# Performance work log

Measured on AMD Instinct MI355X. Metric: run time of the kernel, lower is better.

The kernel has to match this reference:

```python
import jax, jax.numpy as jnp
import numpy as np

H = 8          # num_heads
EPS = 1e-5     # LayerNorm eps (torch default)


def _layernorm(x, gamma, beta):
    mu = jnp.mean(x, axis=-1, keepdims=True)
    var = jnp.mean(jnp.square(x - mu), axis=-1, keepdims=True)
    return (x - mu) * jax.lax.rsqrt(var + EPS) * gamma + beta


def setup_inputs() -> dict:
    key = jax.random.key(0)
    ks = jax.random.split(key, 20)
    B, S, D, F = 32, 1024, 256, 512
    d = D // H
    s = 1.0 / np.sqrt(D)
    sf = 1.0 / np.sqrt(F)
    inp = {
        "x": jax.random.normal(ks[0], (B, S, D), jnp.float32),
        "hidden": jax.random.normal(ks[1], (B, H, S, d), jnp.float32),
        # attention projections (torch Linear layout: [out, in])
        "Wq": jax.random.uniform(ks[2], (D, D), jnp.float32, -s, s),
        "bq": jnp.zeros((D,), jnp.float32),
        "Wk": jax.random.uniform(ks[3], (D, D), jnp.float32, -s, s),
        "bk": jnp.zeros((D,), jnp.float32),
        "Wv": jax.random.uniform(ks[4], (D, D), jnp.float32, -s, s),
        "bv": jnp.zeros((D,), jnp.float32),
        "Wo": jax.random.uniform(ks[5], (D, D), jnp.float32, -s, s),
        "bo": jnp.zeros((D,), jnp.float32),
        # layernorms
        "g1": jnp.ones((D,), jnp.float32),
        "be1": jnp.zeros((D,), jnp.float32),
        "g2": jnp.ones((D,), jnp.float32),
        "be2": jnp.zeros((D,), jnp.float32),
        # feed-forward
        "W1": jax.random.uniform(ks[6], (F, D), jnp.float32, -s, s),
        "b1": jnp.zeros((F,), jnp.float32),
        "W2": jax.random.uniform(ks[7], (D, F), jnp.float32, -sf, sf),
        "b2": jnp.zeros((D,), jnp.float32),
    }
    return inp


def reference(x, hidden, Wq, bq, Wk, bk, Wv, bv, Wo, bo, g1, be1, g2, be2, W1, b1, W2, b2):
    B, S, D = x.shape
    d = D // H
    scale = 1.0 / np.sqrt(d)

    def split_heads(t):  # [B,S,D] -> [B,H,S,d]
        return t.reshape(B, S, H, d).transpose(0, 2, 1, 3)

    q = split_heads(x @ Wq.T + bq)
    k = split_heads(x @ Wk.T + bk)
    v = split_heads(x @ Wv.T + bv)

    # scores with extra hidden-dependent bias: (q k^T + hidden k^T) / sqrt(d)
    scores = jnp.einsum("bhqd,bhkd->bhqk", q, k) * scale
    scores = scores + jnp.einsum("bhqd,bhkd->bhqk", hidden, k) * scale
    attn = jax.nn.softmax(scores, axis=-1)                 # [B,H,S,S]

    ctx = jnp.einsum("bhqk,bhkd->bhqd", attn, v)           # [B,H,S,d]
    ctx = ctx.transpose(0, 2, 1, 3).reshape(B, S, D)
    attn_out = ctx @ Wo.T + bo

    # x = x + x  (note: residual input discarded, attention output doubled)
    h = attn_out + attn_out
    # FFN with residual (dropout is identity at inference)
    h_norm = _layernorm(h, g1, be1)
    ff = jax.nn.relu(h_norm @ W1.T + b1) @ W2.T + b2
    h = h + ff
    # final: x = x + LayerNorm(x)
    h = h + _layernorm(h, g2, be2)
    return (h, attn)
```

## Files before the change

kernel.cpp:

```cpp
#include <hip/hip_runtime.h>

typedef __attribute__((ext_vector_type(8))) short short8;
typedef __attribute__((ext_vector_type(4))) float f32x4;

constexpr int NB  = 32;
constexpr int NS  = 1024;
constexpr int ND  = 256;
constexpr int NH  = 8;
constexpr int NDH = 32;
constexpr int NF  = 512;
constexpr int NM  = NB * NS;
#define RSD 0.17677669529663687f

static __device__ __forceinline__ ushort f2bf(float f) {
    union { float f; unsigned u; } v; v.f = f;
    unsigned r = v.u + 0x7fffu + ((v.u >> 16) & 1u);
    return (ushort)(r >> 16);
}
static __device__ __forceinline__ float bf2f(ushort u) {
    union { unsigned u; float f; } v; v.u = (unsigned)u << 16; return v.f;
}

__global__ __launch_bounds__(256) void split_hi(
    const float* __restrict__ in, ushort* __restrict__ hi, int n4)
{
    int i = blockIdx.x * 256 + threadIdx.x;
    if (i >= n4) return;
    float4 v = ((const float4*)in)[i];
    ushort4 h;
    h.x = f2bf(v.x); h.y = f2bf(v.y); h.z = f2bf(v.z); h.w = f2bf(v.w);
    ((ushort4*)hi)[i] = h;
}

__global__ __launch_bounds__(256) void split_weights(
    const float* __restrict__ Wq, const float* __restrict__ Wk,
    const float* __restrict__ Wv, const float* __restrict__ Wo,
    const float* __restrict__ W1, const float* __restrict__ W2,
    ushort* __restrict__ whi, ushort* __restrict__ wlo)
{
    const int seg = blockIdx.y;
    const float* src;
    size_t off;
    int n4;
    switch (seg) {
        case 0: src = Wq; off = 0;      n4 = 16384; break;
        case 1: src = Wk; off = 65536;  n4 = 16384; break;
        case 2: src = Wv; off = 131072; n4 = 16384; break;
        case 3: src = Wo; off = 196608; n4 = 16384; break;
        case 4: src = W1; off = 262144; n4 = 32768; break;
        default: src = W2; off = 393216; n4 = 32768; break;
    }
    int i = blockIdx.x * 256 + threadIdx.x;
    if (i >= n4) return;
    float4 v = ((const float4*)src)[i];
    ushort4 h, l;
    h.x = f2bf(v.x); l.x = f2bf(v.x - bf2f(h.x));
    h.y = f2bf(v.y); l.y = f2bf(v.y - bf2f(h.y));
    h.z = f2bf(v.z); l.z = f2bf(v.z - bf2f(h.z));
    h.w = f2bf(v.w); l.w = f2bf(v.w - bf2f(h.w));
    ((ushort4*)(whi + off))[i] = h;
    ((ushort4*)(wlo + off))[i] = l;
}

#define GEMM_CORE(K_, TERMS_)                                                  \
    __shared__ ushort sAh[128 * 40], sAl[128 * 40];                            \
    __shared__ ushort sBh[128 * 40], sBl[128 * 40];                            \
    const int t = threadIdx.x;                                                 \
    const int w = t >> 6, ln = t & 63;                                         \
    const int wr = w >> 1, wc = w & 1;                                         \
    const int col = ln & 15, quad = ln >> 4;                                   \
    const int srow = t >> 1, skb = (t & 1) << 4;                               \
    const ushort* gAh = Ahi + (size_t)(rbase + srow) * (K_) + skb;             \
    const ushort* gAl = (TERMS_ == 3) ? Alo + (size_t)(rbase + srow) * (K_) + skb : gAh; \
    const ushort* gBh = Whi + (size_t)(jbase + srow) * (K_) + skb;             \
    const ushort* gBl = Wlo + (size_t)(jbase + srow) * (K_) + skb;             \
    ushort* wAh = &sAh[srow * 40 + skb];                                       \
    ushort* wAl = &sAl[srow * 40 + skb];                                       \
    ushort* wBh = &sBh[srow * 40 + skb];                                       \
    ushort* wBl = &sBl[srow * 40 + skb];                                       \
    f32x4 acc[4][4] = {};                                                      \
    short8 a0 = *(const short8*)(gAh);                                         \
    short8 a1 = *(const short8*)(gAh + 8);                                     \
    short8 c0 = {}, c1 = {};                                                   \
    if (TERMS_ == 3) { c0 = *(const short8*)(gAl); c1 = *(const short8*)(gAl + 8); } \
    short8 b0 = *(const short8*)(gBh);                                         \
    short8 b1 = *(const short8*)(gBh + 8);                                     \
    short8 d0 = *(const short8*)(gBl);                                         \
    short8 d1 = *(const short8*)(gBl + 8);                                     \
    for (int k0 = 0; k0 < (K_); k0 += 32) {                                    \
        __syncthreads();                                                       \
        *(short8*)wAh = a0; *(short8*)(wAh + 8) = a1;                          \
        if (TERMS_ == 3) { *(short8*)wAl = c0; *(short8*)(wAl + 8) = c1; }     \
        *(short8*)wBh = b0; *(short8*)(wBh + 8) = b1;                          \
        *(short8*)wBl = d0; *(short8*)(wBl + 8) = d1;                          \
        __syncthreads();                                                       \
        if (k0 + 32 < (K_)) {                                                  \
            a0 = *(const short8*)(gAh + k0 + 32);                              \
            a1 = *(const short8*)(gAh + k0 + 40);                              \
            if (TERMS_ == 3) {                                                 \
                c0 = *(const short8*)(gAl + k0 + 32);                          \
                c1 = *(const short8*)(gAl + k0 + 40);                          \
            }                                                                  \
            b0 = *(const short8*)(gBh + k0 + 32);                              \
            b1 = *(const short8*)(gBh + k0 + 40);                              \
            d0 = *(const short8*)(gBl + k0 + 32);                              \
            d1 = *(const short8*)(gBl + k0 + 40);                              \
        }                                                                      \
        short8 af[4], afl[4], bfv[4], bfl[4];                                  \
        _Pragma("unroll")                                                      \
        for (int m = 0; m < 4; ++m) {                                          \
            af[m]  = *(const short8*)&sAh[(wr * 64 + m * 16 + col) * 40 + quad * 8]; \
            if (TERMS_ == 3)                                                   \
                afl[m] = *(const short8*)&sAl[(wr * 64 + m * 16 + col) * 40 + quad * 8]; \
            bfv[m] = *(const short8*)&sBh[(wc * 64 + m * 16 + col) * 40 + quad * 8]; \
            bfl[m] = *(const short8*)&sBl[(wc * 64 + m * 16 + col) * 40 + quad * 8]; \
        }                                                                      \
        _Pragma("unroll")                                                      \
        for (int m = 0; m < 4; ++m)                                            \
            _Pragma("unroll")                                                  \
            for (int n = 0; n < 4; ++n) {                                      \
                acc[m][n] = __builtin_amdgcn_mfma_f32_16x16x32_bf16(af[m],  bfv[n], acc[m][n], 0, 0, 0); \
                acc[m][n] = __builtin_amdgcn_mfma_f32_16x16x32_bf16(af[m],  bfl[n], acc[m][n], 0, 0, 0); \
                if (TERMS_ == 3)                                               \
                    acc[m][n] = __builtin_amdgcn_mfma_f32_16x16x32_bf16(afl[m], bfv[n], acc[m][n], 0, 0, 0); \
            }                                                                  \
    }

template<int TERMS>
__global__ __launch_bounds__(256, 2) void gemm_mfma(
    const ushort* __restrict__ Ahi, const ushort* __restrict__ Alo,
    const ushort* __restrict__ Whi, const ushort* __restrict__ Wlo,
    const float* __restrict__ bias,
    float* __restrict__ outf, ushort* __restrict__ ohi,
    int N, int K, int epi)
{
    const int rbase = blockIdx.y << 7;
    const int jbase = blockIdx.x << 7;
    GEMM_CORE(K, TERMS)

    #pragma unroll
    for (int n = 0; n < 4; ++n) {
        const int cg = jbase + wc * 64 + n * 16 + col;
        const float bs = bias[cg];
        #pragma unroll
        for (int m = 0; m < 4; ++m) {
            #pragma unroll
            for (int r = 0; r < 4; ++r) {
                const int row = rbase + wr * 64 + m * 16 + quad * 4 + r;
                float v = acc[m][n][r] + bs;
                size_t oidx = (size_t)row * N + cg;
                if (epi == 0) {
                    outf[oidx] = 2.f * v;
                } else if (epi == 1) {
                    ohi[oidx] = f2bf(fmaxf(v, 0.f));
                } else {
                    outf[oidx] += v;
                }
            }
        }
    }
}

__global__ __launch_bounds__(256, 2) void gemm_qkv_mfma(
    const ushort* __restrict__ xhi,
    const ushort* __restrict__ whi, const ushort* __restrict__ wlo,
    const float* __restrict__ bq, const float* __restrict__ bk, const float* __restrict__ bv,
    const float* __restrict__ hidden,
    ushort* __restrict__ qhi, ushort* __restrict__ qlo,
    ushort* __restrict__ khi, ushort* __restrict__ klo,
    float* __restrict__ vb)
{
    const int z = blockIdx.z;
    const int rbase = blockIdx.y << 7;
    const int jbase = blockIdx.x << 7;
    const ushort* Ahi = xhi;
    const ushort* Alo = xhi;
    const ushort* Whi = whi + (size_t)z * 65536;
    const ushort* Wlo = wlo + (size_t)z * 65536;
    const float* bias = (z == 0) ? bq : (z == 1) ? bk : bv;
    GEMM_CORE(ND, 2)

    #pragma unroll
    for (int n = 0; n < 4; ++n) {
        const int cg = jbase + wc * 64 + n * 16 + col;
        const float bs = bias[cg];
        const int hh = cg >> 5, dd = cg & 31;
        #pragma unroll
        for (int m = 0; m < 4; ++m) {
            #pragma unroll
            for (int r = 0; r < 4; ++r) {
                const int row = rbase + wr * 64 + m * 16 + quad * 4 + r;
                const int b_i = row >> 10, s_i = row & 1023;
                size_t idx = (((size_t)(b_i * NH + hh)) * NS + s_i) * NDH + dd;
                float v = acc[m][n][r] + bs;
                if (z == 2) {
                    vb[idx] = v;
                } else if (z == 0) {
                    v = (v + hidden[idx]) * RSD;
                    ushort h = f2bf(v);
                    qhi[idx] = h;
                    qlo[idx] = f2bf(v - bf2f(h));
                } else {
                    ushort h = f2bf(v);
                    khi[idx] = h;
                    klo[idx] = f2bf(v - bf2f(h));
                }
            }
        }
    }
}

constexpr int VS  = 136;
constexpr int PST = 136;
__global__ __launch_bounds__(256, 4) void attn_flash(
    const ushort* __restrict__ qhi, const ushort* __restrict__ qlo,
    const ushort* __restrict__ khi, const ushort* __restrict__ klo,
    const float* __restrict__ vb,
    float* __restrict__ attn, ushort* __restrict__ cthi, ushort* __restrict__ ctlo)
{
    __shared__ ushort Vthi[32 * VS];
    __shared__ ushort Vtlo[32 * VS];
    __shared__ ushort Ps[4][16 * PST];
    const int bid = blockIdx.x;
    const int lid = (bid & 7) * 512 + (bid >> 3);
    const int qt = lid & 15, bh = lid >> 4;
    const int q0 = qt << 6;
    const int t = threadIdx.x;
    const int w = t >> 6, ln = t & 63;
    const int col = ln & 15, quad = ln >> 4;
    const int qr0 = q0 + 16 * w;
    ushort* myP = Ps[w];

    const size_t bhbase = (size_t)bh * NS * NDH;
    const size_t aoff = bhbase + (size_t)(qr0 + col) * NDH + quad * 8;
    const short8 ahi = *(const short8*)(qhi + aoff);
    const short8 alo = *(const short8*)(qlo + aoff);

    const float* vbase = vb + bhbase;
    const int sdd = t & 31, skg = (t >> 5) << 4;

    f32x4 acc0 = {0.f, 0.f, 0.f, 0.f}, acc1 = {0.f, 0.f, 0.f, 0.f};
    float S[4] = {0.f, 0.f, 0.f, 0.f};

    for (int k0 = 0; k0 < NS; k0 += 128) {
        __syncthreads();
        ushort hs[16], ls[16];
        #pragma unroll
        for (int c = 0; c < 16; ++c) {
            float xx = vbase[(size_t)(k0 + skg + c) * NDH + sdd];
            ushort h = f2bf(xx);
            hs[c] = h; ls[c] = f2bf(xx - bf2f(h));
        }
        #pragma unroll
        for (int c4 = 0; c4 < 4; ++c4) {
            ushort4 hv = make_ushort4(hs[c4 * 4], hs[c4 * 4 + 1], hs[c4 * 4 + 2], hs[c4 * 4 + 3]);
            ushort4 lv = make_ushort4(ls[c4 * 4], ls[c4 * 4 + 1], ls[c4 * 4 + 2], ls[c4 * 4 + 3]);
            *(ushort4*)&Vthi[sdd * VS + skg + c4 * 4] = hv;
            *(ushort4*)&Vtlo[sdd * VS + skg + c4 * 4] = lv;
        }
        __syncthreads();

        #pragma unroll
        for (int tl = 0; tl < 8; ++tl) {
            const int kk = k0 + tl * 16;
            const size_t boff = bhbase + (size_t)(kk + col) * NDH + quad * 8;
            short8 bhi = *(const short8*)(khi + boff);
            short8 blo = *(const short8*)(klo + boff);
            f32x4 c = {0.f, 0.f, 0.f, 0.f};
            c = __builtin_amdgcn_mfma_f32_16x16x32_bf16(ahi, bhi, c, 0, 0, 0);
            c = __builtin_amdgcn_mfma_f32_16x16x32_bf16(ahi, blo, c, 0, 0, 0);
            c = __builtin_amdgcn_mfma_f32_16x16x32_bf16(alo, bhi, c, 0, 0, 0);
            #pragma unroll
            for (int r = 0; r < 4; ++r) {
                float e = __expf(c[r]);
                S[r] += e;
                myP[(quad * 4 + r) * PST + tl * 16 + col] = f2bf(e);
            }
        }

        #pragma unroll
        for (int sl = 0; sl < 4; ++sl) {
            const int kl = sl * 32 + quad * 8;
            short8 pa = *(const short8*)&myP[col * PST + kl];
            short8 bhi0 = *(const short8*)&Vthi[col * VS + kl];
            short8 blo0 = *(const short8*)&Vtlo[col * VS + kl];
            short8 bhi1 = *(const short8*)&Vthi[(16 + col) * VS + kl];
            short8 blo1 = *(const short8*)&Vtlo[(16 + col) * VS + kl];
            acc0 = __builtin_amdgcn_mfma_f32_16x16x32_bf16(pa, bhi0, acc0, 0, 0, 0);
            acc0 = __builtin_amdgcn_mfma_f32_16x16x32_bf16(pa, blo0, acc0, 0, 0, 0);
            acc1 = __builtin_amdgcn_mfma_f32_16x16x32_bf16(pa, bhi1, acc1, 0, 0, 0);
            acc1 = __builtin_amdgcn_mfma_f32_16x16x32_bf16(pa, blo1, acc1, 0, 0, 0);
        }
    }

    float inv[4];
    #pragma unroll
    for (int r = 0; r < 4; ++r) {
        float s = S[r];
        #pragma unroll
        for (int m = 8; m >= 1; m >>= 1) s += __shfl_xor(s, m, 64);
        inv[r] = 1.f / s;
    }

    const int b_i = bh >> 3, hh = bh & 7;
    const int qrow = qr0 + quad * 4;
    #pragma unroll
    for (int r = 0; r < 4; ++r) {
        size_t base = ((size_t)b_i * NS + qrow + r) * ND + hh * NDH;
        float v0 = acc0[r] * inv[r], v1 = acc1[r] * inv[r];
        ushort h0 = f2bf(v0), h1 = f2bf(v1);
        cthi[base + col]      = h0;
        ctlo[base + col]      = f2bf(v0 - bf2f(h0));
        cthi[base + 16 + col] = h1;
        ctlo[base + 16 + col] = f2bf(v1 - bf2f(h1));
    }

    float* abase = attn + ((size_t)bh * NS + qrow) * NS;
    #pragma unroll 4
    for (int tl = 0; tl < 64; ++tl) {
        const int kk = tl * 16;
        const size_t boff = bhbase + (size_t)(kk + col) * NDH + quad * 8;
        short8 bhi = *(const short8*)(khi + boff);
        short8 blo = *(const short8*)(klo + boff);
        f32x4 c = {0.f, 0.f, 0.f, 0.f};
        c = __builtin_amdgcn_mfma_f32_16x16x32_bf16(ahi, bhi, c, 0, 0, 0);
        c = __builtin_amdgcn_mfma_f32_16x16x32_bf16(ahi, blo, c, 0, 0, 0);
        c = __builtin_amdgcn_mfma_f32_16x16x32_bf16(alo, bhi, c, 0, 0, 0);
        #pragma unroll
        for (int r = 0; r < 4; ++r) {
            float p = __expf(c[r]) * inv[r];
            __builtin_nontemporal_store(p, &abase[(size_t)r * NS + kk + col]);
        }
    }
}

__global__ __launch_bounds__(256) void ln_split(
    const float* __restrict__ x, const float* __restrict__ g,
    const float* __restrict__ be, ushort* __restrict__ ohi)
{
    const int t = threadIdx.x;
    const int wave = t >> 6, lane = t & 63;
    const int row = (blockIdx.x << 2) + wave;
    const float* xr = x + (size_t)row * ND;
    float4 v = *(const float4*)&xr[lane << 2];
    float s = v.x + v.y + v.z + v.w;
    #pragma unroll
    for (int m = 32; m >= 1; m >>= 1) s += __shfl_xor(s, m, 64);
    float mu = s * (1.f / 256.f);
    float dx = v.x - mu, dy = v.y - mu, dz = v.z - mu, dw = v.w - mu;
    float s2 = dx * dx + dy * dy + dz * dz + dw * dw;
    #pragma unroll
    for (int m = 32; m >= 1; m >>= 1) s2 += __shfl_xor(s2, m, 64);
    float rs = rsqrtf(s2 * (1.f / 256.f) + 1e-5f);
    float4 gv = *(const float4*)&g[lane << 2];
    float4 bv = *(const float4*)&be[lane << 2];
    ushort4 h;
    h.x = f2bf(dx * rs * gv.x + bv.x);
    h.y = f2bf(dy * rs * gv.y + bv.y);
    h.z = f2bf(dz * rs * gv.z + bv.z);
    h.w = f2bf(dw * rs * gv.w + bv.w);
    ((ushort4*)ohi)[((size_t)row * ND + (lane << 2)) >> 2] = h;
}

__global__ __launch_bounds__(256) void ln_final(
    const float* __restrict__ x, const float* __restrict__ g,
    const float* __restrict__ be, float* __restrict__ out)
{
    const int t = threadIdx.x;
    const int wave = t >> 6, lane = t & 63;
    const int row = (blockIdx.x << 2) + wave;
    const float* xr = x + (size_t)row * ND;
    float4 v = *(const float4*)&xr[lane << 2];
    float s = v.x + v.y + v.z + v.w;
    #pragma unroll
    for (int m = 32; m >= 1; m >>= 1) s += __shfl_xor(s, m, 64);
    float mu = s * (1.f / 256.f);
    float dx = v.x - mu, dy = v.y - mu, dz = v.z - mu, dw = v.w - mu;
    float s2 = dx * dx + dy * dy + dz * dz + dw * dw;
    #pragma unroll
    for (int m = 32; m >= 1; m >>= 1) s2 += __shfl_xor(s2, m, 64);
    float rs = rsqrtf(s2 * (1.f / 256.f) + 1e-5f);
    float4 gv = *(const float4*)&g[lane << 2];
    float4 bv = *(const float4*)&be[lane << 2];
    float4 o;
    o.x = dx * rs * gv.x + bv.x + v.x;
    o.y = dy * rs * gv.y + bv.y + v.y;
    o.z = dz * rs * gv.z + bv.z + v.z;
    o.w = dw * rs * gv.w + bv.w + v.w;
    *(float4*)&out[(size_t)row * ND + (lane << 2)] = o;
}

extern "C" void kernel_launch(void* const* d_in, const int* in_sizes, int n_in,
                              void* d_out, int out_size, void* d_ws, size_t ws_size,
                              hipStream_t stream)
{
    const float* x      = (const float*)d_in[0];
    const float* hidden = (const float*)d_in[1];
    const float* Wq = (const float*)d_in[2];
    const float* bq = (const float*)d_in[3];
    const float* Wk = (const float*)d_in[4];
    const float* bk = (const float*)d_in[5];
    const float* Wv = (const float*)d_in[6];
    const float* bv = (const float*)d_in[7];
    const float* Wo = (const float*)d_in[8];
    const float* bo = (const float*)d_in[9];
    const float* g1  = (const float*)d_in[10];
    const float* be1 = (const float*)d_in[11];
    const float* g2  = (const float*)d_in[12];
    const float* be2 = (const float*)d_in[13];
    const float* W1 = (const float*)d_in[14];
    const float* b1 = (const float*)d_in[15];
    const float* W2 = (const float*)d_in[16];
    const float* b2 = (const float*)d_in[17];

    float* out  = (float*)d_out;
    float* attn = out + (size_t)NM * ND;

    float* ws = (float*)d_ws;
    ushort* xhi  = (ushort*)ws;
    ushort* qhi  = (ushort*)(ws + 8388608);
    ushort* qlo  = (ushort*)(ws + 12582912);
    ushort* khi  = (ushort*)(ws + 16777216);
    ushort* klo  = (ushort*)(ws + 20971520);
    float*  vbuf = ws + 25165824;
    ushort* cthi = (ushort*)ws;
    ushort* ctlo = (ushort*)(ws + 4194304);
    float*  hbuf = ws + 33554432;
    ushort* hnhi = (ushort*)(ws + 8388608);
    ushort* ffhi = (ushort*)(ws + 16777216);
    ushort* whi  = (ushort*)(ws + 41943040);
    ushort* wlo  = (ushort*)(ws + 42205184);

    split_weights<<<dim3(128, 6), 256, 0, stream>>>(Wq, Wk, Wv, Wo, W1, W2, whi, wlo);
    split_hi<<<8192, 256, 0, stream>>>(x, xhi, 2097152);

    gemm_qkv_mfma<<<dim3(2, 256, 3), 256, 0, stream>>>(
        xhi, whi, wlo, bq, bk, bv, hidden, qhi, qlo, khi, klo, vbuf);
    attn_flash<<<dim3(4096), 256, 0, stream>>>(
        qhi, qlo, khi, klo, vbuf, attn, cthi, ctlo);
    gemm_mfma<3><<<dim3(2, 256), 256, 0, stream>>>(
        cthi, ctlo, whi + 196608, wlo + 196608, bo, hbuf, nullptr, ND, ND, 0);
    ln_split<<<NM / 4, 256, 0, stream>>>(hbuf, g1, be1, hnhi);
    gemm_mfma<2><<<dim3(4, 256), 256, 0, stream>>>(
        hnhi, nullptr, whi + 262144, wlo + 262144, b1, nullptr, ffhi, NF, ND, 1);
    gemm_mfma<2><<<dim3(2, 256), 256, 0, stream>>>(
        ffhi, nullptr, whi + 393216, wlo + 393216, b2, hbuf, nullptr, ND, NF, 2);
    ln_final<<<NM / 4, 256, 0, stream>>>(hbuf, g2, be2, out);
}
```

Before: 541.2 us.

## Fuse LayerNorms into output-projection and FFN2 GEMM epilogues

Replaces the O-projection GEMM plus ln_split, and the FFN2 GEMM plus ln_final, with two new GEMM kernels. Each block computes a full 64x256 row tile so the LayerNorm row statistics can be reduced in registers with shuffles. This removes two elementwise kernels and their round trips of the hidden buffer through global memory. In exchange, each kernel launches only 512 blocks with large accumulator arrays and bigger shared tiles, which may lower occupancy. Variance now uses E[x²]-mu², which is less accurate than the previous two-pass form.

Result: faster. 525.3 us (-2.9%).

```diff
diff --git a/kernel.cpp b/kernel.cpp
--- a/kernel.cpp
+++ b/kernel.cpp
@@ -210,6 +210,189 @@
     }
 }
 
+__global__ __launch_bounds__(256, 2) void gemm_oproj_ln(
+    const ushort* __restrict__ Ahi, const ushort* __restrict__ Alo,
+    const ushort* __restrict__ Whi, const ushort* __restrict__ Wlo,
+    const float* __restrict__ bias, const float* __restrict__ g,
+    const float* __restrict__ be,
+    float* __restrict__ hbuf, ushort* __restrict__ hnhi)
+{
+    __shared__ ushort sAh[64 * 40], sAl[64 * 40];
+    __shared__ ushort sBh[256 * 40], sBl[256 * 40];
+    const int t = threadIdx.x;
+    const int w = t >> 6, ln = t & 63;
+    const int col = ln & 15, quad = ln >> 4;
+    const int rbase = blockIdx.x << 6;
+    const int arow = t >> 2, akb = (t & 3) << 3;
+    const ushort* gAh = Ahi + (size_t)(rbase + arow) * ND + akb;
+    const ushort* gAl = Alo + (size_t)(rbase + arow) * ND + akb;
+    const ushort* gBh = Whi + (size_t)t * ND;
+    const ushort* gBl = Wlo + (size_t)t * ND;
+    ushort* wAh = &sAh[arow * 40 + akb];
+    ushort* wAl = &sAl[arow * 40 + akb];
+    ushort* wBh = &sBh[t * 40];
+    ushort* wBl = &sBl[t * 40];
+
+    f32x4 acc[16] = {};
+    short8 a0 = *(const short8*)gAh;
+    short8 c0 = *(const short8*)gAl;
+    short8 b0 = *(const short8*)(gBh),      b1 = *(const short8*)(gBh + 8);
+    short8 b2v = *(const short8*)(gBh + 16), b3 = *(const short8*)(gBh + 24);
+    short8 d0 = *(const short8*)(gBl),      d1 = *(const short8*)(gBl + 8);
+    short8 d2v = *(const short8*)(gBl + 16), d3 = *(const short8*)(gBl + 24);
+
+    for (int k0 = 0; k0 < ND; k0 += 32) {
+        __syncthreads();
+        *(short8*)wAh = a0; *(short8*)wAl = c0;
+        *(short8*)(wBh + 0) = b0;  *(short8*)(wBh + 8) = b1;
+        *(short8*)(wBh + 16) = b2v; *(short8*)(wBh + 24) = b3;
+        *(short8*)(wBl + 0) = d0;  *(short8*)(wBl + 8) = d1;
+        *(short8*)(wBl + 16) = d2v; *(short8*)(wBl + 24) = d3;
+        __syncthreads();
+        if (k0 + 32 < ND) {
+            a0 = *(const short8*)(gAh + k0 + 32);
+            c0 = *(const short8*)(gAl + k0 + 32);
+            b0 = *(const short8*)(gBh + k0 + 32); b1 = *(const short8*)(gBh + k0 + 40);
+            b2v = *(const short8*)(gBh + k0 + 48); b3 = *(const short8*)(gBh + k0 + 56);
+            d0 = *(const short8*)(gBl + k0 + 32); d1 = *(const short8*)(gBl + k0 + 40);
+            d2v = *(const short8*)(gBl + k0 + 48); d3 = *(const short8*)(gBl + k0 + 56);
+        }
+        short8 af  = *(const short8*)&sAh[(w * 16 + col) * 40 + quad * 8];
+        short8 afl = *(const short8*)&sAl[(w * 16 + col) * 40 + quad * 8];
+        #pragma unroll
+        for (int n = 0; n < 16; ++n) {
+            short8 bv = *(const short8*)&sBh[(n * 16 + col) * 40 + quad * 8];
+            short8 bl = *(const short8*)&sBl[(n * 16 + col) * 40 + quad * 8];
+            acc[n] = __builtin_amdgcn_mfma_f32_16x16x32_bf16(af,  bv, acc[n], 0, 0, 0);
+            acc[n] = __builtin_amdgcn_mfma_f32_16x16x32_bf16(af,  bl, acc[n], 0, 0, 0);
+            acc[n] = __builtin_amdgcn_mfma_f32_16x16x32_bf16(afl, bv, acc[n], 0, 0, 0);
+        }
+    }
+
+    const int row0 = rbase + w * 16 + quad * 4;
+    float s[4] = {}, s2[4] = {};
+    #pragma unroll
+    for (int n = 0; n < 16; ++n) {
+        float bs = bias[n * 16 + col];
+        #pragma unroll
+        for (int r = 0; r < 4; ++r) {
+            float hv = 2.f * (acc[n][r] + bs);
+            acc[n][r] = hv;
+            s[r] += hv; s2[r] += hv * hv;
+            hbuf[(size_t)(row0 + r) * ND + n * 16 + col] = hv;
+        }
+    }
+    float mu[4], rsd[4];
+    #pragma unroll
+    for (int r = 0; r < 4; ++r) {
+        #pragma unroll
+        for (int m = 8; m >= 1; m >>= 1) {
+            s[r]  += __shfl_xor(s[r],  m, 64);
+            s2[r] += __shfl_xor(s2[r], m, 64);
+        }
+        mu[r] = s[r] * (1.f / 256.f);
+        float var = s2[r] * (1.f / 256.f) - mu[r] * mu[r];
+        rsd[r] = rsqrtf(var + 1e-5f);
+    }
+    #pragma unroll
+    for (int n = 0; n < 16; ++n) {
+        float gv = g[n * 16 + col], bv = be[n * 16 + col];
+        #pragma unroll
+        for (int r = 0; r < 4; ++r)
+            hnhi[(size_t)(row0 + r) * ND + n * 16 + col] =
+                f2bf((acc[n][r] - mu[r]) * rsd[r] * gv + bv);
+    }
+}
+
+__global__ __launch_bounds__(256, 2) void gemm_ffn2_ln(
+    const ushort* __restrict__ Ahi,
+    const ushort* __restrict__ Whi, const ushort* __restrict__ Wlo,
+    const float* __restrict__ bias, const float* __restrict__ g,
+    const float* __restrict__ be,
+    const float* __restrict__ hbuf, float* __restrict__ out)
+{
+    __shared__ ushort sAh[64 * 40];
+    __shared__ ushort sBh[256 * 40], sBl[256 * 40];
+    const int t = threadIdx.x;
+    const int w = t >> 6, ln = t & 63;
+    const int col = ln & 15, quad = ln >> 4;
+    const int rbase = blockIdx.x << 6;
+    const int arow = t >> 2, akb = (t & 3) << 3;
+    const ushort* gAh = Ahi + (size_t)(rbase + arow) * NF + akb;
+    const ushort* gBh = Whi + (size_t)t * NF;
+    const ushort* gBl = Wlo + (size_t)t * NF;
+    ushort* wAh = &sAh[arow * 40 + akb];
+    ushort* wBh = &sBh[t * 40];
+    ushort* wBl = &sBl[t * 40];
+
+    f32x4 acc[16] = {};
+    short8 a0 = *(const short8*)gAh;
+    short8 b0 = *(const short8*)(gBh),      b1 = *(const short8*)(gBh + 8);
+    short8 b2v = *(const short8*)(gBh + 16), b3 = *(const short8*)(gBh + 24);
+    short8 d0 = *(const short8*)(gBl),      d1 = *(const short8*)(gBl + 8);
+    short8 d2v = *(const short8*)(gBl + 16), d3 = *(const short8*)(gBl + 24);
+
+    for (int k0 = 0; k0 < NF; k0 += 32) {
+        __syncthreads();
+        *(short8*)wAh = a0;
+        *(short8*)(wBh + 0) = b0;  *(short8*)(wBh + 8) = b1;
+        *(short8*)(wBh + 16) = b2v; *(short8*)(wBh + 24) = b3;
+        *(short8*)(wBl + 0) = d0;  *(short8*)(wBl + 8) = d1;
+        *(short8*)(wBl + 16) = d2v; *(short8*)(wBl + 24) = d3;
+        __syncthreads();
+        if (k0 + 32 < NF) {
+            a0 = *(const short8*)(gAh + k0 + 32);
+            b0 = *(const short8*)(gBh + k0 + 32); b1 = *(const short8*)(gBh + k0 + 40);
+            b2v = *(const short8*)(gBh + k0 + 48); b3 = *(const short8*)(gBh + k0 + 56);
+            d0 = *(const short8*)(gBl + k0 + 32); d1 = *(const short8*)(gBl + k0 + 40);
+            d2v = *(const short8*)(gBl + k0 + 48); d3 = *(const short8*)(gBl + k0 + 56);
+        }
+        short8 af = *(const short8*)&sAh[(w * 16 + col) * 40 + quad * 8];
+        #pragma unroll
+        for (int n = 0; n < 16; ++n) {
+            short8 bv = *(const short8*)&sBh[(n * 16 + col) * 40 + quad * 8];
+            short8 bl = *(const short8*)&sBl[(n * 16 + col) * 40 + quad * 8];
+            acc[n] = __builtin_amdgcn_mfma_f32_16x16x32_bf16(af, bv, acc[n], 0, 0, 0);
+            acc[n] = __builtin_amdgcn_mfma_f32_16x16x32_bf16(af, bl, acc[n], 0, 0, 0);
+        }
+    }
+
+    const int row0 = rbase + w * 16 + quad * 4;
+    float s[4] = {}, s2[4] = {};
+    #pragma unroll
+    for (int n = 0; n < 16; ++n) {
+        float bs = bias[n * 16 + col];
+        #pragma unroll
+        for (int r = 0; r < 4; ++r) {
+            float hv = hbuf[(size_t)(row0 + r) * ND + n * 16 + col] + acc[n][r] + bs;
+            acc[n][r] = hv;
+            s[r] += hv; s2[r] += hv * hv;
+        }
+    }
+    float mu[4], rsd[4];
+    #pragma unroll
+    for (int r = 0; r < 4; ++r) {
+        #pragma unroll
+        for (int m = 8; m >= 1; m >>= 1) {
+            s[r]  += __shfl_xor(s[r],  m, 64);
+            s2[r] += __shfl_xor(s2[r], m, 64);
+        }
+        mu[r] = s[r] * (1.f / 256.f);
+        float var = s2[r] * (1.f / 256.f) - mu[r] * mu[r];
+        rsd[r] = rsqrtf(var + 1e-5f);
+    }
+    #pragma unroll
+    for (int n = 0; n < 16; ++n) {
+        float gv = g[n * 16 + col], bv = be[n * 16 + col];
+        #pragma unroll
+        for (int r = 0; r < 4; ++r) {
+            float hv = acc[n][r];
+            out[(size_t)(row0 + r) * ND + n * 16 + col] =
+                hv + (hv - mu[r]) * rsd[r] * gv + bv;
+        }
+    }
+}
+
 constexpr int VS  = 136;
 constexpr int PST = 136;
 __global__ __launch_bounds__(256, 4) void attn_flash(
@@ -332,62 +515,6 @@
             __builtin_nontemporal_store(p, &abase[(size_t)r * NS + kk + col]);
         }
     }
-}
-
-__global__ __launch_bounds__(256) void ln_split(
-    const float* __restrict__ x, const float* __restrict__ g,
-    const float* __restrict__ be, ushort* __restrict__ ohi)
-{
-    const int t = threadIdx.x;
-    const int wave = t >> 6, lane = t & 63;
-    const int row = (blockIdx.x << 2) + wave;
-    const float* xr = x + (size_t)row * ND;
-    float4 v = *(const float4*)&xr[lane << 2];
-    float s = v.x + v.y + v.z + v.w;
-    #pragma unroll
-    for (int m = 32; m >= 1; m >>= 1) s += __shfl_xor(s, m, 64);
-    float mu = s * (1.f / 256.f);
-    float dx = v.x - mu, dy = v.y - mu, dz = v.z - mu, dw = v.w - mu;
-    float s2 = dx * dx + dy * dy + dz * dz + dw * dw;
-    #pragma unroll
-    for (int m = 32; m >= 1; m >>= 1) s2 += __shfl_xor(s2, m, 64);
-    float rs = rsqrtf(s2 * (1.f / 256.f) + 1e-5f);
-    float4 gv = *(const float4*)&g[lane << 2];
-    float4 bv = *(const float4*)&be[lane << 2];
-    ushort4 h;
-    h.x = f2bf(dx * rs * gv.x + bv.x);
-    h.y = f2bf(dy * rs * gv.y + bv.y);
-    h.z = f2bf(dz * rs * gv.z + bv.z);
-    h.w = f2bf(dw * rs * gv.w + bv.w);
-    ((ushort4*)ohi)[((size_t)row * ND + (lane << 2)) >> 2] = h;
-}
-
-__global__ __launch_bounds__(256) void ln_final(
-    const float* __restrict__ x, const float* __restrict__ g,
-    const float* __restrict__ be, float* __restrict__ out)
-{
-    const int t = threadIdx.x;
-    const int wave = t >> 6, lane = t & 63;
-    const int row = (blockIdx.x << 2) + wave;
-    const float* xr = x + (size_t)row * ND;
-    float4 v = *(const float4*)&xr[lane << 2];
-    float s = v.x + v.y + v.z + v.w;
-    #pragma unroll
-    for (int m = 32; m >= 1; m >>= 1) s += __shfl_xor(s, m, 64);
-    float mu = s * (1.f / 256.f);
-    float dx = v.x - mu, dy = v.y - mu, dz = v.z - mu, dw = v.w - mu;
-    float s2 = dx * dx + dy * dy + dz * dz + dw * dw;
-    #pragma unroll
-    for (int m = 32; m >= 1; m >>= 1) s2 += __shfl_xor(s2, m, 64);
-    float rs = rsqrtf(s2 * (1.f / 256.f) + 1e-5f);
-    float4 gv = *(const float4*)&g[lane << 2];
-    float4 bv = *(const float4*)&be[lane << 2];
-    float4 o;
-    o.x = dx * rs * gv.x + bv.x + v.x;
-    o.y = dy * rs * gv.y + bv.y + v.y;
-    o.z = dz * rs * gv.z + bv.z + v.z;
-    o.w = dw * rs * gv.w + bv.w + v.w;
-    *(float4*)&out[(size_t)row * ND + (lane << 2)] = o;
 }
 
 extern "C" void kernel_launch(void* const* d_in, const int* in_sizes, int n_in,
@@ -438,12 +565,10 @@
         xhi, whi, wlo, bq, bk, bv, hidden, qhi, qlo, khi, klo, vbuf);
     attn_flash<<<dim3(4096), 256, 0, stream>>>(
         qhi, qlo, khi, klo, vbuf, attn, cthi, ctlo);
-    gemm_mfma<3><<<dim3(2, 256), 256, 0, stream>>>(
-        cthi, ctlo, whi + 196608, wlo + 196608, bo, hbuf, nullptr, ND, ND, 0);
-    ln_split<<<NM / 4, 256, 0, stream>>>(hbuf, g1, be1, hnhi);
+    gemm_oproj_ln<<<dim3(NM / 64), 256, 0, stream>>>(
+        cthi, ctlo, whi + 196608, wlo + 196608, bo, g1, be1, hbuf, hnhi);
     gemm_mfma<2><<<dim3(4, 256), 256, 0, stream>>>(
         hnhi, nullptr, whi + 262144, wlo + 262144, b1, nullptr, ffhi, NF, ND, 1);
-    gemm_mfma<2><<<dim3(2, 256), 256, 0, stream>>>(
-        ffhi, nullptr, whi + 393216, wlo + 393216, b2, hbuf, nullptr, ND, NF, 2);
-    ln_final<<<NM / 4, 256, 0, stream>>>(hbuf, g2, be2, out);
-}
+    gemm_ffn2_ln<<<dim3(NM / 64), 256, 0, stream>>>(
+        ffhi, whi + 393216, wlo + 393216, b2, g2, be2, hbuf, out);
+}
```
